# Optimization experiments

Measured on AMD Instinct MI355X. Metric: run time of the kernel, lower is better.

The kernel has to match this reference:

```python
import jax, jax.numpy as jnp
import numpy as np
from jax import lax

H = W = 128            # feature map spatial size (2h x 2w)
WIN = 16               # attention window size
DIM = 512
HEADS = 8
DIM_HEAD = 64
INNER = HEADS * DIM_HEAD
SCALE = DIM_HEAD ** -0.5
KEEP = 44
IOU_T = 0.2

_s = np.arange(0, H - WIN + 1, WIN // 2)
_sx, _sy = np.meshgrid(_s, _s)
WINDOWS = np.stack([_sx.ravel(), _sy.ravel(), _sx.ravel() + WIN - 1, _sy.ravel() + WIN - 1], 1).astype(np.float32)
M = WINDOWS.shape[0]   # 225
SX = jnp.asarray(WINDOWS[:, 0].astype(np.int32))
SY = jnp.asarray(WINDOWS[:, 1].astype(np.int32))

# ---- static pairwise IoU (torchvision convention: area=(x2-x1)*(y2-y1)) ----
_x1, _y1, _x2, _y2 = WINDOWS[:, 0], WINDOWS[:, 1], WINDOWS[:, 2], WINDOWS[:, 3]
_area = (_x2 - _x1) * (_y2 - _y1)
_iw = np.clip(np.minimum(_x2[:, None], _x2[None]) - np.maximum(_x1[:, None], _x1[None]), 0, None)
_ih = np.clip(np.minimum(_y2[:, None], _y2[None]) - np.maximum(_y1[:, None], _y1[None]), 0, None)
_inter = _iw * _ih
IOU = jnp.asarray((_inter / (_area[:, None] + _area[None] - _inter)).astype(np.float32))

# ---- roi_align (aligned=False, 1 sample/bin) == separable bilinear resample ----
_bin = (WIN - 1.0) / WIN
_r = (np.arange(WIN) + 0.5) * _bin
_q = np.floor(_r).astype(int)
_f = _r - _q
_A = np.zeros((WIN, WIN), np.float32)
_A[np.arange(WIN), _q] = 1.0 - _f
_A[np.arange(WIN), np.minimum(_q + 1, WIN - 1)] += _f
BILIN = jnp.asarray(_A)


def _nms_select(score):
    """Greedy NMS over the static window set; return first KEEP kept indices."""
    order = jnp.argsort(-score)
    iou_s = IOU[order][:, order]
    def body(i, supp):
        return supp | ((~supp[i]) & (iou_s[i] > IOU_T) & (jnp.arange(M) > i))
    supp = lax.fori_loop(0, M, body, jnp.zeros((M,), dtype=bool))
    pos = jnp.where(~supp, jnp.arange(M), M)
    pos = jnp.minimum(jnp.sort(pos)[:KEEP], M - 1)
    return order[pos]


def setup_inputs() -> dict:
    key = jax.random.key(0)
    k1, k2, k3, k4 = jax.random.split(key, 4)
    x = jax.random.normal(k1, (8, H * W, DIM), dtype=jnp.float32)
    prob = jax.random.uniform(k2, (8, 4, H // 2, W // 2), dtype=jnp.float32)
    W_fix = jnp.ones((1, 1, WIN // 2, WIN // 2), jnp.float32)   # FixCNN ones kernel
    W_qkv = jax.random.normal(k3, (3 * INNER, DIM), jnp.float32) * 0.02
    W_out = jax.random.normal(k4, (DIM, INNER), jnp.float32) * 0.02
    b_out = jnp.zeros((DIM,), jnp.float32)
    return {"x": x, "prob": prob, "W_fix": W_fix, "W_qkv": W_qkv, "W_out": W_out, "b_out": b_out}


def reference(x, prob, W_fix, W_qkv, W_out, b_out):
    b = x.shape[0]
    # entropy over class channels
    entropy = -jnp.sum(prob * jnp.log2(prob + 1e-10), axis=1)           # (b, 64, 64)
    # FixCNN: ones 8x8 kernel, stride 4, then /64
    score = lax.conv(entropy[:, None], W_fix, (WIN // 4, WIN // 4), 'VALID')
    score = (score / float((WIN // 2) ** 2)).reshape(b, -1)             # (b, M)
    x2d = x.transpose(0, 2, 1).reshape(b, DIM, H, W)                    # b d h w
    rng = jnp.arange(WIN)

    def per_batch(feat, sc):
        idx = _nms_select(sc)                                           # (KEEP,)
        sy, sx = SY[idx], SX[idx]
        # gather integer 16x16 patches (box corners are integers)
        patches = jax.vmap(lambda y, xc: lax.dynamic_slice(feat, (0, y, xc), (DIM, WIN, WIN)))(sy, sx)
        # roi_align bilinear resample (separable)
        pat = jnp.einsum('pi,mdij,qj->mdpq', BILIN, patches, BILIN)     # (KEEP, d, 16, 16)
        xi = pat.transpose(0, 2, 3, 1).reshape(KEEP, WIN * WIN, DIM)    # m n d
        qkv = xi @ W_qkv.T
        q, k, v = jnp.split(qkv, 3, axis=-1)
        to_h = lambda t: t.reshape(KEEP, WIN * WIN, HEADS, DIM_HEAD).transpose(0, 2, 1, 3)
        q, k, v = to_h(q), to_h(k), to_h(v)
        attn = jax.nn.softmax(jnp.einsum('mhnd,mhkd->mhnk', q, k) * SCALE, axis=-1)
        out = jnp.einsum('mhnk,mhkd->mhnd', attn, v)
        out = out.transpose(0, 2, 1, 3).reshape(KEEP, WIN * WIN, INNER)
        out = out @ W_out.T + b_out                                     # (KEEP, n, DIM)
        out2d = out.reshape(KEEP, WIN, WIN, DIM).transpose(0, 3, 1, 2)  # m d h w
        yy = sy[:, None, None] + rng[None, :, None]                     # (KEEP,16,1)
        xx = sx[:, None, None] + rng[None, None, :]                     # (KEEP,1,16)
        acc = jnp.zeros((DIM, H, W), x.dtype).at[:, yy, xx].add(out2d.transpose(1, 0, 2, 3))
        cnt = jnp.zeros((H, W), x.dtype).at[yy, xx].add(1.0)
        return acc, cnt

    acc, cnt = jax.vmap(per_batch)(x2d, score)
    outx = (acc / (cnt[:, None] + 1e-10)).reshape(b, DIM, H * W).transpose(0, 2, 1)
    return x + outx
```

## Files before the change

### kernel.cpp

```cpp
#include <hip/hip_runtime.h>
#include <type_traits>
#include <utility>

typedef unsigned short u16;
typedef __attribute__((ext_vector_type(8))) short short8;
typedef __attribute__((ext_vector_type(8))) __bf16 bf16v8;
typedef __attribute__((ext_vector_type(4))) float f32x4;
typedef __attribute__((ext_vector_type(16))) float f32x16;

template <typename T, typename = void> struct mfma_ok : std::false_type {};
template <typename T>
struct mfma_ok<T, std::void_t<decltype(__builtin_amdgcn_mfma_f32_16x16x32_bf16(
    std::declval<T>(), std::declval<T>(), std::declval<f32x4>(), 0, 0, 0))>>
    : std::true_type {};
using frag8 = std::conditional_t<mfma_ok<bf16v8>::value, bf16v8, short8>;

#define MFMA16(a, b, c) __builtin_amdgcn_mfma_f32_16x16x32_bf16((a), (b), (c), 0, 0, 0)
#define MFMA32(a, b, c) __builtin_amdgcn_mfma_f32_32x32x16_bf16((a), (b), (c), 0, 0, 0)

__device__ __forceinline__ float bf2f(u16 u) {
  unsigned v = ((unsigned)u) << 16;
  return __builtin_bit_cast(float, v);
}
__device__ __forceinline__ u16 f2bf(float f) {
  unsigned u = __builtin_bit_cast(unsigned, f);
  u = (u + 0x7fffu + ((u >> 16) & 1u)) >> 16;
  return (u16)u;
}
__device__ __forceinline__ unsigned cvtpk_bf16(float lo, float hi) {
  unsigned r;
  asm("v_cvt_pk_bf16_f32 %0, %1, %2" : "=v"(r) : "v"(lo), "v"(hi));
  return r;
}
__device__ __forceinline__ void gl16(const u16* g, u16* l) {
  __builtin_amdgcn_global_load_lds((__attribute__((address_space(1))) void*)(g),
                                   (__attribute__((address_space(3))) void*)(l), 16, 0, 0);
}
__device__ __forceinline__ void vmw8() { asm volatile("s_waitcnt vmcnt(8)" ::: "memory"); }
__device__ __forceinline__ void vmw0() { asm volatile("s_waitcnt vmcnt(0)" ::: "memory"); }
__device__ __forceinline__ void lgw0() { asm volatile("s_waitcnt lgkmcnt(0)" ::: "memory"); }


__global__ void k_score(const float* __restrict__ prob, const float* __restrict__ wfix,
                        float* __restrict__ scores) {
  const int b = blockIdx.x, tid = threadIdx.x;
  __shared__ float ent[64 * 64];
  __shared__ float wf[64];
  if (tid < 64) wf[tid] = wfix[tid];
  const float* pb = prob + (size_t)b * 4 * 4096;
  for (int p = tid; p < 4096; p += 256) {
    float e = 0.f;
#pragma unroll
    for (int ch = 0; ch < 4; ++ch) {
      float v = pb[ch * 4096 + p];
      e -= v * log2f(v + 1e-10f);
    }
    ent[p] = e;
  }
  __syncthreads();
  if (tid < 225) {
    int wy = tid / 15, wx = tid % 15;
    float s = 0.f;
    for (int a = 0; a < 8; ++a)
      for (int c = 0; c < 8; ++c)
        s += ent[(wy * 4 + a) * 64 + wx * 4 + c] * wf[a * 8 + c];
    scores[b * 225 + tid] = s * (1.0f / 64.0f);
  }
}

__device__ __forceinline__ float iou_pair(int wa, int wb) {
  float x1a = (float)((wa % 15) * 8), y1a = (float)((wa / 15) * 8);
  float x1b = (float)((wb % 15) * 8), y1b = (float)((wb / 15) * 8);
  float iw = fminf(x1a, x1b) + 15.f - fmaxf(x1a, x1b);
  float ih = fminf(y1a, y1b) + 15.f - fmaxf(y1a, y1b);
  iw = fmaxf(iw, 0.f);
  ih = fmaxf(ih, 0.f);
  float inter = iw * ih;
  return inter / (450.f - inter);
}

__global__ void k_nms(const float* __restrict__ scores, int* __restrict__ sel,
                      int* __restrict__ kept, float* __restrict__ mult) {
  const int b = blockIdx.x, t = threadIdx.x;
  __shared__ float s[225];
  __shared__ int order[225];
  __shared__ unsigned char supp[225];
  __shared__ int idx44[44];
  __shared__ int ks[225];
  __shared__ float ml[225];
  if (t < 225) s[t] = scores[b * 225 + t];
  __syncthreads();
  if (t < 225) {
    float st = s[t];
    int r = 0;
    for (int j = 0; j < 225; ++j) {
      float sj = s[j];
      r += (sj > st) || (sj == st && j < t);
    }
    order[r] = t;
    supp[t] = 0;
    ks[t] = -1;
    ml[t] = 0.f;
  }
  __syncthreads();
  for (int i = 0; i < 224; ++i) {
    if (t > i && t < 225 && !supp[i]) {
      if (iou_pair(order[i], order[t]) > 0.2f) supp[t] = 1;
    }
    __syncthreads();
  }
  if (t == 0) {
    int k = 0;
    for (int i = 0; i < 225 && k < 44; ++i)
      if (!supp[i]) idx44[k++] = order[i];
    while (k < 44) idx44[k++] = order[224];
    for (int k2 = 0; k2 < 44; ++k2) {
      int w = idx44[k2];
      if (ks[w] < 0) ks[w] = k2;
      ml[w] += 1.f;
    }
  }
  __syncthreads();
  if (t < 225) {
    kept[b * 225 + t] = ks[t];
    mult[b * 225 + t] = ml[t];
  }
  if (t < 44) sel[b * 44 + t] = idx44[t];
}

__global__ void k_castw(const float* __restrict__ Wq, const float* __restrict__ Wo,
                        u16* __restrict__ wqb, u16* __restrict__ wob) {
  int idx = blockIdx.x * 256 + threadIdx.x;
  if (idx < 786432) wqb[idx] = f2bf(Wq[idx]);
  int i2 = idx - 786432;
  if (i2 >= 0 && i2 < 262144) wob[i2] = f2bf(Wo[i2]);
}

__global__ __launch_bounds__(256) void k_gather(const float* __restrict__ x,
                                                const int* __restrict__ sel,
                                                u16* __restrict__ xi) {
  const size_t idx = (size_t)blockIdx.x * 256 + threadIdx.x;
  const int dc = (int)(idx & 63);
  const int pq = (int)((idx >> 6) & 255);
  const int g = (int)(idx >> 14);
  const int b = g / 44;
  const int w = sel[g];
  const int sy = (w / 15) * 8, sx = (w % 15) * 8;
  const int p = pq >> 4, q = pq & 15;
  float rp = ((float)p + 0.5f) * 0.9375f;
  int i0 = (int)rp;
  float fp = rp - (float)i0;
  float rq = ((float)q + 0.5f) * 0.9375f;
  int j0 = (int)rq;
  float fq = rq - (float)j0;
  const float w00 = (1.f - fp) * (1.f - fq), w01 = (1.f - fp) * fq;
  const float w10 = fp * (1.f - fq), w11 = fp * fq;
  const float* xb = x + ((size_t)b * 16384 + (size_t)(sy + i0) * 128 + sx + j0) * 512 + dc * 8;
  const float4* t00 = (const float4*)xb;
  const float4* t01 = (const float4*)(xb + 512);
  const float4* t10 = (const float4*)(xb + 512 * 128);
  const float4* t11 = (const float4*)(xb + 512 * 129);
  float acc[8];
#pragma unroll
  for (int h = 0; h < 2; ++h) {
    float4 a = t00[h], bb = t01[h], c = t10[h], d = t11[h];
    acc[h * 4 + 0] = w00 * a.x + w01 * bb.x + w10 * c.x + w11 * d.x;
    acc[h * 4 + 1] = w00 * a.y + w01 * bb.y + w10 * c.y + w11 * d.y;
    acc[h * 4 + 2] = w00 * a.z + w01 * bb.z + w10 * c.z + w11 * d.z;
    acc[h * 4 + 3] = w00 * a.w + w01 * bb.w + w10 * c.w + w11 * d.w;
  }
  short8 o;
#pragma unroll
  for (int e = 0; e < 8; ++e) o[e] = (short)f2bf(acc[e]);
  *(short8*)&xi[((size_t)g * 256 + pq) * 512 + dc * 8] = o;
}

template <int BIAS, int OPERM, int APERM>
__global__ __launch_bounds__(256, 2) void k_gemm128(const u16* __restrict__ A,
                                                    const u16* __restrict__ B, u16* __restrict__ C,
                                                    const float* __restrict__ bias, int M, int N,
                                                    int K, int nbn) {
  __shared__ u16 smem[32768];
  u16* sA = smem;
  u16* sB = smem + 16384;
  const int tid = threadIdx.x, lane = tid & 63, wv = tid >> 6;
  const int f = blockIdx.x;
  const int q8 = gridDim.x >> 3;
  const int wg = (f & 7) * q8 + (f >> 3);
  const int bm = wg / nbn, bn = wg % nbn;
  const int wm = (wv >> 1) * 64, wn = (wv & 1) * 64;
  const int l15 = lane & 15, k8 = (lane >> 4) * 8;
  const int xorv = (l15 & 7) * 8;
  const int srow = tid >> 3;
  const int sc8 = ((tid ^ (tid >> 3)) & 7) * 8;
  const int arow0 = bm * 128 + srow, brow0 = bn * 128 + srow;

  f32x4 acc[4][4] = {};

#define STAGE(kt, buf)                                                                      \
  {                                                                                         \
    _Pragma("unroll") for (int c = 0; c < 4; ++c) {                                         \
      const int ar = arow0 + c * 32;                                                        \
      size_t aoffs = APERM ? ((size_t)(ar >> 8) * 131072 + (size_t)(kt) * 16384 +           \
                              (size_t)(ar & 255) * 64 + sc8)                                \
                           : ((size_t)ar * K + (kt) * 64 + sc8);                            \
      gl16(A + aoffs, &sA[(buf) * 8192 + c * 2048 + wv * 512]);                             \
      gl16(B + (size_t)(brow0 + c * 32) * K + (kt) * 64 + sc8,                              \
           &sB[(buf) * 8192 + c * 2048 + wv * 512]);                                        \
    }                                                                                       \
  }

  STAGE(0, 0);
  STAGE(1, 1);

  for (int t = 0; t < 8; ++t) {
    const int buf = t & 1;
    if (t == 7)
      vmw0();
    else
      vmw8();
    __builtin_amdgcn_sched_barrier(0);
    __builtin_amdgcn_s_barrier();
    frag8 af[4][2], bf[4][2];
#pragma unroll
    for (int i = 0; i < 4; ++i)
#pragma unroll
      for (int kk = 0; kk < 2; ++kk) {
        af[i][kk] =
            *(const frag8*)&sA[buf * 8192 + (wm + i * 16 + l15) * 64 + ((kk * 32 + k8) ^ xorv)];
        bf[i][kk] =
            *(const frag8*)&sB[buf * 8192 + (wn + i * 16 + l15) * 64 + ((kk * 32 + k8) ^ xorv)];
      }
    __builtin_amdgcn_s_setprio(1);
#pragma unroll
    for (int i = 0; i < 4; ++i)
#pragma unroll
      for (int j = 0; j < 4; ++j)
#pragma unroll
        for (int kk = 0; kk < 2; ++kk)
          acc[i][j] = MFMA16(af[i][kk], bf[j][kk], acc[i][j]);
    __builtin_amdgcn_s_setprio(0);
    lgw0();
    __builtin_amdgcn_sched_barrier(0);
    __builtin_amdgcn_s_barrier();
    if (t < 6) STAGE(t + 2, buf);
  }
#undef STAGE

  const int cc = lane & 15, rr = (lane >> 4) * 4;
  u16* sc = smem + wv * 4352;
#pragma unroll
  for (int i = 0; i < 4; ++i)
#pragma unroll
    for (int j = 0; j < 4; ++j) {
      int cloc = j * 16 + cc;
      float badd = BIAS ? bias[bn * 128 + wn + cloc] : 0.f;
#pragma unroll
      for (int e = 0; e < 4; ++e)
        sc[(i * 16 + rr + e) * 68 + cloc] = f2bf(acc[i][j][e] + badd);
    }
  asm volatile("" ::: "memory");
  const int row0 = bm * 128 + wm, col0 = bn * 128 + wn;
  u16* Cb;
  size_t rstride;
  if (OPERM) {
    Cb = C + (size_t)(row0 >> 8) * 393216 + (size_t)(col0 >> 9) * 131072 +
         (size_t)((col0 >> 6) & 7) * 16384 + (size_t)(row0 & 255) * 64;
    rstride = 64;
  } else {
    Cb = C + (size_t)row0 * N + col0;
    rstride = (size_t)N;
  }
#pragma unroll
  for (int rep = 0; rep < 8; ++rep) {
    int r = rep * 8 + (lane >> 3);
    int c8 = (lane & 7) * 8;
    uint2 lo = *(const uint2*)&sc[r * 68 + c8];
    uint2 hi = *(const uint2*)&sc[r * 68 + c8 + 4];
    *(int4*)&Cb[(size_t)r * rstride + c8] = make_int4((int)lo.x, (int)lo.y, (int)hi.x, (int)hi.y);
  }
}

__global__ __launch_bounds__(256, 4) void k_attn(const u16* __restrict__ qkv,
                                                 u16* __restrict__ aout) {
  const int g = blockIdx.x;
  const int win = g % 352;
  const int hq = g / 352;
  const int h = hq & 7, qh = hq >> 3;
  const int tid = threadIdx.x, lane = tid & 63, wv = tid >> 6;
  const int l31 = lane & 31, l5 = lane >> 5;
  __shared__ u16 smem[8832];
  u16* KbB = smem;
  u16* VtB = smem + 4352;
  const u16* qbase = qkv + (size_t)win * 393216 + (size_t)h * 16384;
  const u16* kbase = qbase + 131072;
  const u16* vbase = qbase + 262144;
  const int prow = tid >> 2, pc16 = (tid & 3) * 16;
  const int qrow0 = qh * 128 + wv * 32;

  frag8 qf[4];
#pragma unroll
  for (int c = 0; c < 4; ++c)
    qf[c] = *(const frag8*)(qbase + (size_t)(qrow0 + l31) * 64 + c * 16 + l5 * 8);

  f32x16 of[2] = {};
  float m_run = -3e38f;
  float l_run = 0.f;

  for (int kb = 0; kb < 4; ++kb) {
    __syncthreads();
    {
      const u16* kp = kbase + (size_t)(kb * 64 + prow) * 64 + pc16;
      short8 ka = *(const short8*)kp;
      short8 kb2 = *(const short8*)(kp + 8);
      const u16* vp = vbase + (size_t)(kb * 64 + prow) * 64 + pc16;
      short8 va = *(const short8*)vp;
      short8 vb2 = *(const short8*)(vp + 8);
      *(short8*)&KbB[prow * 68 + pc16] = ka;
      *(short8*)&KbB[prow * 68 + pc16 + 8] = kb2;
#pragma unroll
      for (int e = 0; e < 8; ++e) {
        VtB[(pc16 + e) * 70 + prow] = (u16)va[e];
        VtB[(pc16 + 8 + e) * 70 + prow] = (u16)vb2[e];
      }
    }
    __syncthreads();
    f32x16 s0 = {}, s1 = {};
#pragma unroll
    for (int c = 0; c < 4; ++c) {
      frag8 kf0 = *(const frag8*)&KbB[l31 * 68 + c * 16 + l5 * 8];
      frag8 kf1 = *(const frag8*)&KbB[(32 + l31) * 68 + c * 16 + l5 * 8];
      s0 = MFMA32(kf0, qf[c], s0);
      s1 = MFMA32(kf1, qf[c], s1);
    }
    float tm[16];
#pragma unroll
    for (int r = 0; r < 16; ++r) tm[r] = fmaxf(s0[r], s1[r]);
#pragma unroll
    for (int r = 0; r < 8; ++r) tm[r] = fmaxf(tm[r], tm[r + 8]);
#pragma unroll
    for (int r = 0; r < 4; ++r) tm[r] = fmaxf(tm[r], tm[r + 4]);
    float pm = fmaxf(fmaxf(tm[0], tm[1]), fmaxf(tm[2], tm[3]));
    pm = fmaxf(pm, __shfl_xor(pm, 32));
    if (!__all(pm <= m_run + 64.f)) {
      float mn = fmaxf(m_run, pm);
      float corr = __expf((m_run - mn) * 0.125f);
      l_run *= corr;
#pragma unroll
      for (int dt = 0; dt < 2; ++dt)
#pragma unroll
        for (int r = 0; r < 16; ++r) of[dt][r] *= corr;
      m_run = mn;
    }
    const float mqt = m_run;
    float ls = 0.f;
#pragma unroll
    for (int kt = 0; kt < 2; ++kt) {
      const f32x16 sv = kt ? s1 : s0;
      float p[16];
#pragma unroll
      for (int r = 0; r < 16; ++r) p[r] = __expf((sv[r] - mqt) * 0.125f);
      float e0 = (p[0] + p[1]) + (p[2] + p[3]);
      float e1 = (p[4] + p[5]) + (p[6] + p[7]);
      float e2 = (p[8] + p[9]) + (p[10] + p[11]);
      float e3 = (p[12] + p[13]) + (p[14] + p[15]);
      ls += (e0 + e1) + (e2 + e3);
#pragma unroll
      for (int cc = 0; cc < 2; ++cc) {
        const int bx = cc * 8;
        unsigned a0 = cvtpk_bf16(p[bx + 0], p[bx + 1]);
        unsigned a1 = cvtpk_bf16(p[bx + 2], p[bx + 3]);
        unsigned b0 = cvtpk_bf16(p[bx + 4], p[bx + 5]);
        unsigned b1 = cvtpk_bf16(p[bx + 6], p[bx + 7]);
        asm("v_permlane32_swap_b32 %0, %1" : "+v"(a0), "+v"(b0));
        asm("v_permlane32_swap_b32 %0, %1" : "+v"(a1), "+v"(b1));
        uint4 fu;
        fu.x = a0;
        fu.y = a1;
        fu.z = b0;
        fu.w = b1;
        frag8 pb = __builtin_bit_cast(frag8, fu);
#pragma unroll
        for (int dt = 0; dt < 2; ++dt) {
          frag8 va = *(const frag8*)&VtB[(dt * 32 + l31) * 70 + kt * 32 + cc * 16 + l5 * 8];
          of[dt] = MFMA32(va, pb, of[dt]);
        }
      }
    }
    l_run += ls;
  }

  float lt = l_run + __shfl_xor(l_run, 32);
  float inv = 1.0f / lt;
  u16* sc = smem + wv * 2176;
  __syncthreads();
#pragma unroll
  for (int dt = 0; dt < 2; ++dt)
#pragma unroll
    for (int j = 0; j < 4; ++j) {
      unsigned w0 = cvtpk_bf16(of[dt][4 * j + 0] * inv, of[dt][4 * j + 1] * inv);
      unsigned w1 = cvtpk_bf16(of[dt][4 * j + 2] * inv, of[dt][4 * j + 3] * inv);
      *(uint2*)&sc[l31 * 68 + dt * 32 + 8 * j + 4 * l5] = make_uint2(w0, w1);
    }
  asm volatile("" ::: "memory");
  u16* obase = aout + (size_t)win * 131072 + (size_t)h * 16384 + (size_t)qrow0 * 64;
#pragma unroll
  for (int rep = 0; rep < 4; ++rep) {
    int row = rep * 8 + (lane >> 3);
    uint2 lo = *(const uint2*)&sc[row * 68 + (lane & 7) * 8];
    uint2 hi = *(const uint2*)&sc[row * 68 + (lane & 7) * 8 + 4];
    *(int4*)&obase[(size_t)row * 64 + (lane & 7) * 8] =
        make_int4((int)lo.x, (int)lo.y, (int)hi.x, (int)hi.y);
  }
}

__global__ void k_final(const float* __restrict__ x, const u16* __restrict__ proj,
                        const int* __restrict__ kept, const float* __restrict__ mult,
                        float* __restrict__ out) {
  const size_t idx = (size_t)blockIdx.x * 256 + threadIdx.x;
  const int dci = (int)(idx & 31);
  const int pix = (int)((idx >> 5) & 16383);
  const int b = (int)(idx >> 19);
  const int y = pix >> 7, xc = pix & 127;
  float acc[16];
#pragma unroll
  for (int e = 0; e < 16; ++e) acc[e] = 0.f;
  float c = 0.f;
  const int wyh = y >> 3, wxh = xc >> 3;
#pragma unroll
  for (int a = 0; a < 2; ++a) {
    int wy = wyh - 1 + a;
    if (wy < 0 || wy > 14) continue;
#pragma unroll
    for (int bb = 0; bb < 2; ++bb) {
      int wx = wxh - 1 + bb;
      if (wx < 0 || wx > 14) continue;
      int w = wy * 15 + wx;
      int slot = kept[b * 225 + w];
      if (slot < 0) continue;
      float ml = mult[b * 225 + w];
      c += ml;
      const u16* pr = proj +
                      ((size_t)((b * 44 + slot) * 256 + (y - wy * 8) * 16 + (xc - wx * 8))) * 512 +
                      (size_t)dci * 16;
      short8 v0 = *(const short8*)pr;
      short8 v1 = *(const short8*)(pr + 8);
#pragma unroll
      for (int e = 0; e < 8; ++e) acc[e] += ml * bf2f((u16)v0[e]);
#pragma unroll
      for (int e = 0; e < 8; ++e) acc[8 + e] += ml * bf2f((u16)v1[e]);
    }
  }
  const float inv = 1.f / (c + 1e-10f);
  const size_t off = ((size_t)(b * 16384 + pix)) * 512 + (size_t)dci * 16;
  const float4* xp = (const float4*)(x + off);
  float4* op = (float4*)(out + off);
#pragma unroll
  for (int q4 = 0; q4 < 4; ++q4) {
    float4 xv = xp[q4];
    float4 ov;
    ov.x = xv.x + acc[q4 * 4 + 0] * inv;
    ov.y = xv.y + acc[q4 * 4 + 1] * inv;
    ov.z = xv.z + acc[q4 * 4 + 2] * inv;
    ov.w = xv.w + acc[q4 * 4 + 3] * inv;
    op[q4] = ov;
  }
}

extern "C" void kernel_launch(void* const* d_in, const int* in_sizes, int n_in, void* d_out,
                              int out_size, void* d_ws, size_t ws_size, hipStream_t stream) {
  const float* x = (const float*)d_in[0];
  const float* prob = (const float*)d_in[1];
  const float* wfix = (const float*)d_in[2];
  const float* Wq = (const float*)d_in[3];
  const float* Wo = (const float*)d_in[4];
  const float* bo = (const float*)d_in[5];
  float* out = (float*)d_out;
  char* ws = (char*)d_ws;

  float* scores = (float*)(ws + 0);
  int* sel = (int*)(ws + 8192);
  int* kept = (int*)(ws + 16384);
  float* mult = (float*)(ws + 24576);
  u16* wqb = (u16*)(ws + 32768);
  u16* wob = (u16*)(ws + 32768 + 1572864);
  u16* xi = (u16*)(ws + 4194304);
  u16* qkv = (u16*)(ws + 4194304 + 92274688);
  u16* aout = xi;
  u16* proj = qkv;

  k_score<<<8, 256, 0, stream>>>(prob, wfix, scores);
  k_nms<<<8, 256, 0, stream>>>(scores, sel, kept, mult);
  k_castw<<<4096, 256, 0, stream>>>(Wq, Wo, wqb, wob);
  k_gather<<<22528, 256, 0, stream>>>(x, sel, xi);
  k_gemm128<0, 1, 0><<<8448, 256, 0, stream>>>(xi, wqb, qkv, nullptr, 90112, 1536, 512, 12);
  k_attn<<<5632, 256, 0, stream>>>(qkv, aout);
  k_gemm128<1, 0, 1><<<2816, 256, 0, stream>>>(aout, wob, proj, bo, 90112, 512, 512, 4);
  k_final<<<16384, 256, 0, stream>>>(x, proj, kept, mult, out);
}
```

Measured before the change: 698.4 us.

## Load full window K/V once per block and cover all queries with 8 waves

The attention kernel now uses 512-thread blocks that handle all 256 queries of a window-head. It stages the full K and transposed V (256 rows) into shared memory once, up front. Previously, two query-half blocks each re-read K/V in four 64-row chunks with two barriers per chunk. This halves global K/V traffic and removes the per-iteration synchronisation. In exchange, shared memory per block rises to about 68KB, which can limit how many blocks fit on a CU, and the V transpose store pattern changes.

```diff
diff --git a/kernel.cpp b/kernel.cpp
--- a/kernel.cpp
+++ b/kernel.cpp
@@ -281,55 +281,53 @@
   }
 }
 
-__global__ __launch_bounds__(256, 4) void k_attn(const u16* __restrict__ qkv,
+__global__ __launch_bounds__(512, 4) void k_attn(const u16* __restrict__ qkv,
                                                  u16* __restrict__ aout) {
   const int g = blockIdx.x;
-  const int win = g % 352;
-  const int hq = g / 352;
-  const int h = hq & 7, qh = hq >> 3;
+  const int win = g % 352, h = g / 352;
   const int tid = threadIdx.x, lane = tid & 63, wv = tid >> 6;
   const int l31 = lane & 31, l5 = lane >> 5;
-  __shared__ u16 smem[8832];
+  __shared__ u16 smem[34176];
   u16* KbB = smem;
-  u16* VtB = smem + 4352;
+  u16* VtB = smem + 17408;
   const u16* qbase = qkv + (size_t)win * 393216 + (size_t)h * 16384;
   const u16* kbase = qbase + 131072;
   const u16* vbase = qbase + 262144;
-  const int prow = tid >> 2, pc16 = (tid & 3) * 16;
-  const int qrow0 = qh * 128 + wv * 32;
+  const int qrow0 = wv * 32;
 
   frag8 qf[4];
 #pragma unroll
   for (int c = 0; c < 4; ++c)
     qf[c] = *(const frag8*)(qbase + (size_t)(qrow0 + l31) * 64 + c * 16 + l5 * 8);
+  {
+    const int srow = tid >> 1, kcol = (tid & 1) * 32;
+    const u16* kp = kbase + (size_t)srow * 64 + kcol;
+    const u16* vp = vbase + (size_t)srow * 64 + kcol;
+    short8 kv[4], vv[4];
+#pragma unroll
+    for (int c4 = 0; c4 < 4; ++c4) {
+      kv[c4] = *(const short8*)(kp + c4 * 8);
+      vv[c4] = *(const short8*)(vp + c4 * 8);
+    }
+#pragma unroll
+    for (int c4 = 0; c4 < 4; ++c4) *(short8*)&KbB[srow * 68 + kcol + c4 * 8] = kv[c4];
+#pragma unroll
+    for (int c4 = 0; c4 < 4; ++c4)
+#pragma unroll
+      for (int e = 0; e < 8; ++e) VtB[(kcol + c4 * 8 + e) * 262 + srow] = (u16)vv[c4][e];
+  }
+  __syncthreads();
 
   f32x16 of[2] = {};
   float m_run = -3e38f;
   float l_run = 0.f;
 
   for (int kb = 0; kb < 4; ++kb) {
-    __syncthreads();
-    {
-      const u16* kp = kbase + (size_t)(kb * 64 + prow) * 64 + pc16;
-      short8 ka = *(const short8*)kp;
-      short8 kb2 = *(const short8*)(kp + 8);
-      const u16* vp = vbase + (size_t)(kb * 64 + prow) * 64 + pc16;
-      short8 va = *(const short8*)vp;
-      short8 vb2 = *(const short8*)(vp + 8);
-      *(short8*)&KbB[prow * 68 + pc16] = ka;
-      *(short8*)&KbB[prow * 68 + pc16 + 8] = kb2;
-#pragma unroll
-      for (int e = 0; e < 8; ++e) {
-        VtB[(pc16 + e) * 70 + prow] = (u16)va[e];
-        VtB[(pc16 + 8 + e) * 70 + prow] = (u16)vb2[e];
-      }
-    }
-    __syncthreads();
     f32x16 s0 = {}, s1 = {};
 #pragma unroll
     for (int c = 0; c < 4; ++c) {
-      frag8 kf0 = *(const frag8*)&KbB[l31 * 68 + c * 16 + l5 * 8];
-      frag8 kf1 = *(const frag8*)&KbB[(32 + l31) * 68 + c * 16 + l5 * 8];
+      frag8 kf0 = *(const frag8*)&KbB[(kb * 64 + l31) * 68 + c * 16 + l5 * 8];
+      frag8 kf1 = *(const frag8*)&KbB[(kb * 64 + 32 + l31) * 68 + c * 16 + l5 * 8];
       s0 = MFMA32(kf0, qf[c], s0);
       s1 = MFMA32(kf1, qf[c], s1);
     }
@@ -382,7 +380,8 @@
         frag8 pb = __builtin_bit_cast(frag8, fu);
 #pragma unroll
         for (int dt = 0; dt < 2; ++dt) {
-          frag8 va = *(const frag8*)&VtB[(dt * 32 + l31) * 70 + kt * 32 + cc * 16 + l5 * 8];
+          frag8 va =
+              *(const frag8*)&VtB[(dt * 32 + l31) * 262 + kb * 64 + kt * 32 + cc * 16 + l5 * 8];
           of[dt] = MFMA32(va, pb, of[dt]);
         }
       }
@@ -494,7 +493,7 @@
   k_castw<<<4096, 256, 0, stream>>>(Wq, Wo, wqb, wob);
   k_gather<<<22528, 256, 0, stream>>>(x, sel, xi);
   k_gemm128<0, 1, 0><<<8448, 256, 0, stream>>>(xi, wqb, qkv, nullptr, 90112, 1536, 512, 12);
-  k_attn<<<5632, 256, 0, stream>>>(qkv, aout);
+  k_attn<<<2816, 512, 0, stream>>>(qkv, aout);
   k_gemm128<1, 0, 1><<<2816, 256, 0, stream>>>(aout, wob, proj, bo, 90112, 512, 512, 4);
   k_final<<<16384, 256, 0, stream>>>(x, proj, kept, mult, out);
 }
```

After: 692.0 us, median of 2. About the same (-0.9%).
